# Kernel optimization log

Hardware: AMD Instinct MI355X
Metric: run time of the kernel (lower is better)

Reference implementation:

```python
import jax, jax.numpy as jnp
import numpy as np

N_NODES = 100000
N_EDGES = 800000
VOCAB = 100
D_FEAT = 10
D = 64
EPS = 1e-8  # torch F.cosine_similarity eps


def setup_inputs() -> dict:
    key = jax.random.key(0)
    ks = jax.random.split(key, 8)
    return {
        "nodes": jax.random.randint(ks[0], (N_NODES,), 0, VOCAB),
        "edges": jax.random.randint(ks[1], (N_EDGES, 2), 0, N_NODES),
        "features": jax.random.normal(ks[2], (N_NODES, D_FEAT), dtype=jnp.float32),
        "node_emb": jax.random.normal(ks[3], (VOCAB, D), dtype=jnp.float32),
        "feat_W": jax.random.normal(ks[4], (D, D_FEAT), dtype=jnp.float32) * 0.1,
        "feat_b": jnp.zeros((D,), dtype=jnp.float32),
        "conv1_W": jax.random.normal(ks[5], (D, D), dtype=jnp.float32) * 0.1,
        "conv1_b": jnp.zeros((D,), dtype=jnp.float32),
        "pattern_emb": jax.random.normal(ks[6], (VOCAB, D), dtype=jnp.float32),
        "pattern_id": 42,  # hash(node_type) % 100
    }


def reference(nodes, edges, features, node_emb, feat_W, feat_b,
              conv1_W, conv1_b, pattern_emb, pattern_id):
    # initial embeddings: type embedding + linear feature projection  [N, D]
    embeds = node_emb[nodes] + (features @ feat_W.T + feat_b)

    src, dst = edges[:, 0], edges[:, 1]
    for _ in range(2):  # fixed 2 message-passing rounds (structural loop)
        # scatter-add messages from src to dst (order-independent sum)
        agg = jnp.zeros_like(embeds).at[dst].add(embeds[src])
        embeds = jax.nn.relu((embeds + agg) @ conv1_W.T + conv1_b)

    # cosine similarity of each node embedding against the pattern embedding
    p = pattern_emb[pattern_id]  # [D]
    num = embeds @ p  # [N]
    denom = jnp.maximum(jnp.linalg.norm(embeds, axis=1), EPS) * \
            jnp.maximum(jnp.linalg.norm(p), EPS)
    return num / denom  # [N] match scores
```

## Files before the change

### kernel.cpp

```cpp
#include <hip/hip_runtime.h>
#include <hip/hip_bf16.h>

#define N_NODES 100000
#define N_EDGES 800000
#define D 64
#define SCAN_B 256
#define NB1 ((N_NODES + SCAN_B - 1) / SCAN_B)
#define FILL_BLOCKS (N_EDGES / 256)
#define INIT_BLOCKS (N_NODES * D / 256)
#define CT 64
#define XS 68
#define OS 72

__device__ __forceinline__ unsigned short f2bf(float f) {
    union { float f; unsigned u; } v; v.f = f;
    unsigned r = v.u + 0x7fffu + ((v.u >> 16) & 1u);
    return (unsigned short)(r >> 16);
}
__device__ __forceinline__ float bf2f(unsigned short u) {
    return __uint_as_float(((unsigned)u) << 16);
}
__device__ __forceinline__ void acc_bf8(float acc[8], uint4 u) {
    acc[0] += __uint_as_float(u.x << 16);
    acc[1] += __uint_as_float(u.x & 0xffff0000u);
    acc[2] += __uint_as_float(u.y << 16);
    acc[3] += __uint_as_float(u.y & 0xffff0000u);
    acc[4] += __uint_as_float(u.z << 16);
    acc[5] += __uint_as_float(u.z & 0xffff0000u);
    acc[6] += __uint_as_float(u.w << 16);
    acc[7] += __uint_as_float(u.w & 0xffff0000u);
}
__device__ __forceinline__ unsigned pack2bf(float a, float b) {
    return (unsigned)f2bf(a) | ((unsigned)f2bf(b) << 16);
}

__global__ __launch_bounds__(256) void hist_rank_kernel(
        const int2* __restrict__ edges,
        int* __restrict__ deg,
        int* __restrict__ rank) {
    int t = blockIdx.x * 256 + threadIdx.x;
    int2 e = edges[t];
    rank[t] = atomicAdd(&deg[e.y], 1);
}

__global__ void scan1_kernel(const int* __restrict__ deg,
                             int* __restrict__ row_ptr,
                             int* __restrict__ bsum) {
    __shared__ int tmp[SCAN_B];
    int t = threadIdx.x;
    int i = blockIdx.x * SCAN_B + t;
    int v = (i < N_NODES) ? deg[i] : 0;
    tmp[t] = v;
    __syncthreads();
#pragma unroll
    for (int off = 1; off < SCAN_B; off <<= 1) {
        int a = (t >= off) ? tmp[t - off] : 0;
        __syncthreads();
        tmp[t] += a;
        __syncthreads();
    }
    if (i < N_NODES) row_ptr[i] = tmp[t] - v;
    if (t == SCAN_B - 1) bsum[blockIdx.x] = tmp[t];
}

__global__ void scan23_kernel(int* __restrict__ row_ptr,
                              const int* __restrict__ bsum) {
    __shared__ int red[SCAN_B];
    int t = threadIdx.x;
    int partial = 0;
    if (t < blockIdx.x && t < NB1) partial += bsum[t];
    int t2 = t + 256;
    if (t2 < blockIdx.x && t2 < NB1) partial += bsum[t2];
    red[t] = partial;
    __syncthreads();
#pragma unroll
    for (int off = 128; off > 0; off >>= 1) {
        if (t < off) red[t] += red[t + off];
        __syncthreads();
    }
    int boff = red[0];
    int i = blockIdx.x * SCAN_B + t;
    if (i < N_NODES) row_ptr[i] += boff;
    if (i == 0) row_ptr[N_NODES] = N_EDGES;
}

__global__ __launch_bounds__(256) void fill_init_kernel(
        const int2* __restrict__ edges,
        const int* __restrict__ rank,
        const int* __restrict__ rowp,
        int* __restrict__ col,
        const int* __restrict__ nodes,
        const float* __restrict__ features,
        const float* __restrict__ node_emb,
        const float* __restrict__ feat_W,
        const float* __restrict__ feat_b,
        unsigned short* __restrict__ embeds) {
    if (blockIdx.x < FILL_BLOCKS) {
        int t = blockIdx.x * 256 + threadIdx.x;
        int2 e = edges[t];
        col[rowp[e.y] + rank[t]] = e.x;
    } else {
        int tid = (blockIdx.x - FILL_BLOCKS) * 256 + threadIdx.x;
        int node = tid >> 6;
        int d = tid & 63;
        float acc = feat_b[d];
        const float* f = features + (size_t)node * 10;
        const float* w = feat_W + (size_t)d * 10;
#pragma unroll
        for (int j = 0; j < 10; ++j) acc += f[j] * w[j];
        embeds[tid] = f2bf(node_emb[(size_t)nodes[node] * D + d] + acc);
    }
}

__global__ __launch_bounds__(256, 8) void gather_x_kernel(
        const unsigned short* __restrict__ emb_in,
        const int* __restrict__ rowp,
        const int* __restrict__ col,
        unsigned short* __restrict__ x_out) {
    int lane = threadIdx.x & 63;
    int wv   = threadIdx.x >> 6;
    int node = blockIdx.x * 4 + wv;
    int g = lane >> 3;
    int c = lane & 7;

    int start = rowp[node];
    int end   = rowp[node + 1];

    float acc[8];
#pragma unroll
    for (int j = 0; j < 8; ++j) acc[j] = 0.f;
    if (g == 0) {
        uint4 u = ((const uint4*)(emb_in + (size_t)node * D))[c];
        acc_bf8(acc, u);
    }

    for (int base = start; base < end; base += 32) {
        int nb = end - base; if (nb > 32) nb = 32;
        int idx = (lane < nb) ? col[base + lane] : 0;
#pragma unroll
        for (int r = 0; r < 4; ++r) {
            int s = r * 8 + g;
            int src = __shfl(idx, s, 64);
            if (s < nb) {
                uint4 u = ((const uint4*)(emb_in + (size_t)src * D))[c];
                acc_bf8(acc, u);
            }
        }
    }

#pragma unroll
    for (int m = 8; m <= 32; m <<= 1) {
#pragma unroll
        for (int j = 0; j < 8; ++j) acc[j] += __shfl_xor(acc[j], m, 64);
    }

    if (g == 0) {
        uint4 p;
        p.x = pack2bf(acc[0], acc[1]);
        p.y = pack2bf(acc[2], acc[3]);
        p.z = pack2bf(acc[4], acc[5]);
        p.w = pack2bf(acc[6], acc[7]);
        ((uint4*)(x_out + (size_t)node * D))[c] = p;
    }
}

template <bool SCORE>
__global__ __launch_bounds__(256) void conv_tile_kernel(
        const unsigned short* __restrict__ x,
        const float* __restrict__ W,
        const float* __restrict__ b,
        const float* __restrict__ pattern_emb,
        const int* __restrict__ pattern_id,
        unsigned short* __restrict__ emb_out,
        float* __restrict__ score_out) {
    __shared__ float Xs[CT][XS];
    __shared__ float Wsh[D][XS];
    __shared__ unsigned short Os[CT][OS];
    __shared__ float ps[D];

    int t = threadIdx.x;
    int base = blockIdx.x * CT;
    int i = t & 15;
    int j = t >> 4;

    float bj[4];
#pragma unroll
    for (int dj = 0; dj < 4; ++dj) bj[dj] = b[j + 16 * dj];

    {
        int c = t & 15;
        int r0 = t >> 4;
#pragma unroll
        for (int p4 = 0; p4 < 4; ++p4) {
            int r = r0 + p4 * 16;
            float4 wv4 = ((const float4*)(W + (size_t)r * D))[c];
            *((float4*)&Wsh[r][4 * c]) = wv4;
        }
    }
#pragma unroll
    for (int q = 0; q < 2; ++q) {
        int idx = t + q * 256;
        int r = idx >> 3, ck = idx & 7;
        int node = base + r;
        int nc = node < N_NODES ? node : (N_NODES - 1);
        uint4 u = ((const uint4*)(x + (size_t)nc * D))[ck];
        float4 a, bb;
        a.x  = bf2f((unsigned short)(u.x & 0xffff)); a.y  = bf2f((unsigned short)(u.x >> 16));
        a.z  = bf2f((unsigned short)(u.y & 0xffff)); a.w  = bf2f((unsigned short)(u.y >> 16));
        bb.x = bf2f((unsigned short)(u.z & 0xffff)); bb.y = bf2f((unsigned short)(u.z >> 16));
        bb.z = bf2f((unsigned short)(u.w & 0xffff)); bb.w = bf2f((unsigned short)(u.w >> 16));
        *((float4*)&Xs[r][8 * ck])     = a;
        *((float4*)&Xs[r][8 * ck + 4]) = bb;
    }
    if (SCORE && t < D) ps[t] = pattern_emb[(size_t)pattern_id[0] * D + t];
    __syncthreads();

    float acc[4][4] = {};
    for (int k4 = 0; k4 < 16; ++k4) {
        float4 xr[4], wr[4];
#pragma unroll
        for (int di = 0; di < 4; ++di) xr[di] = *((const float4*)&Xs[i + 16 * di][4 * k4]);
#pragma unroll
        for (int dj = 0; dj < 4; ++dj) wr[dj] = *((const float4*)&Wsh[j + 16 * dj][4 * k4]);
#pragma unroll
        for (int di = 0; di < 4; ++di)
#pragma unroll
            for (int dj = 0; dj < 4; ++dj)
                acc[di][dj] += xr[di].x * wr[dj].x + xr[di].y * wr[dj].y
                             + xr[di].z * wr[dj].z + xr[di].w * wr[dj].w;
    }

    if (!SCORE) {
#pragma unroll
        for (int di = 0; di < 4; ++di)
#pragma unroll
            for (int dj = 0; dj < 4; ++dj)
                Os[i + 16 * di][j + 16 * dj] = f2bf(fmaxf(acc[di][dj] + bj[dj], 0.f));
        __syncthreads();
#pragma unroll
        for (int q = 0; q < 2; ++q) {
            int idx = t + q * 256;
            int r = idx >> 3, seg = idx & 7;
            int node = base + r;
            if (node < N_NODES)
                ((uint4*)(emb_out + (size_t)node * D))[seg] = *((const uint4*)&Os[r][8 * seg]);
        }
    } else {
        __syncthreads();
#pragma unroll
        for (int di = 0; di < 4; ++di)
#pragma unroll
            for (int dj = 0; dj < 4; ++dj)
                Xs[i + 16 * di][j + 16 * dj] = fmaxf(acc[di][dj] + bj[dj], 0.f);
        __syncthreads();
        if (t < CT) {
            float dot = 0.f, n2 = 0.f, pn = 0.f;
#pragma unroll 8
            for (int k = 0; k < D; ++k) {
                float yk = Xs[t][k];
                float pk = ps[k];
                dot += yk * pk; n2 += yk * yk; pn += pk * pk;
            }
            int node = base + t;
            if (node < N_NODES)
                score_out[node] = dot / (fmaxf(sqrtf(n2), 1e-8f) * fmaxf(sqrtf(pn), 1e-8f));
        }
    }
}

__global__ void init_embeds_kernel(const int* __restrict__ nodes,
                                   const float* __restrict__ features,
                                   const float* __restrict__ node_emb,
                                   const float* __restrict__ feat_W,
                                   const float* __restrict__ feat_b,
                                   float* __restrict__ embeds) {
    int tid = blockIdx.x * blockDim.x + threadIdx.x;
    if (tid >= N_NODES * D) return;
    int node = tid >> 6;
    int d = tid & 63;
    float acc = feat_b[d];
    const float* f = features + (size_t)node * 10;
    const float* w = feat_W + (size_t)d * 10;
#pragma unroll
    for (int j = 0; j < 10; ++j) acc += f[j] * w[j];
    embeds[tid] = node_emb[(size_t)nodes[node] * D + d] + acc;
}

__global__ void scatter_add_kernel(const int* __restrict__ edges,
                                   const float* __restrict__ embeds,
                                   float* __restrict__ agg) {
    int tid = blockIdx.x * blockDim.x + threadIdx.x;
    int edge = tid >> 6;
    int lane = tid & 63;
    if (edge >= N_EDGES) return;
    int src = edges[2 * edge + 0];
    int dst = edges[2 * edge + 1];
    atomicAdd(&agg[(size_t)dst * D + lane], embeds[(size_t)src * D + lane]);
}

__global__ void conv_inplace_kernel(const float* __restrict__ agg,
                                    const float* __restrict__ W,
                                    const float* __restrict__ b,
                                    float* __restrict__ embeds) {
    __shared__ float Ws[D * 65];
    __shared__ float xs[4][D];
    for (int i = threadIdx.x; i < D * D; i += blockDim.x) {
        int d = i >> 6, k = i & 63;
        Ws[d * 65 + k] = W[i];
    }
    __syncthreads();
    int lane_d = threadIdx.x & 63;
    int local_n = threadIdx.x >> 6;
    float bias = b[lane_d];
    const int n_chunks = (N_NODES + 3) / 4;
    for (int chunk = blockIdx.x; chunk < n_chunks; chunk += gridDim.x) {
        int node = chunk * 4 + local_n;
        if (node < N_NODES) {
            size_t base = (size_t)node * D + lane_d;
            xs[local_n][lane_d] = embeds[base] + agg[base];
        }
        __syncthreads();
        if (node < N_NODES) {
            float acc = bias;
#pragma unroll
            for (int k = 0; k < D; ++k) acc += xs[local_n][k] * Ws[lane_d * 65 + k];
            embeds[(size_t)node * D + lane_d] = fmaxf(acc, 0.0f);
        }
        __syncthreads();
    }
}

__global__ void final_score_kernel(const float* __restrict__ embeds,
                                   const float* __restrict__ pattern_emb,
                                   const int* __restrict__ pattern_id,
                                   float* __restrict__ out) {
    int lane = threadIdx.x & 63;
    int wave = threadIdx.x >> 6;
    int node = blockIdx.x * 4 + wave;
    int pid = pattern_id[0];
    float p = pattern_emb[(size_t)pid * D + lane];
    float pn = p * p;
#pragma unroll
    for (int m = 32; m > 0; m >>= 1) pn += __shfl_xor(pn, m, 64);
    if (node < N_NODES) {
        float e = embeds[(size_t)node * D + lane];
        float dot = e * p;
        float n2 = e * e;
#pragma unroll
        for (int m = 32; m > 0; m >>= 1) {
            dot += __shfl_xor(dot, m, 64);
            n2  += __shfl_xor(n2, m, 64);
        }
        if (lane == 0) {
            float denom = fmaxf(sqrtf(n2), 1e-8f) * fmaxf(sqrtf(pn), 1e-8f);
            out[node] = dot / denom;
        }
    }
}

extern "C" void kernel_launch(void* const* d_in, const int* in_sizes, int n_in,
                              void* d_out, int out_size, void* d_ws, size_t ws_size,
                              hipStream_t stream) {
    const int*   nodes       = (const int*)d_in[0];
    const int*   edges       = (const int*)d_in[1];
    const float* features    = (const float*)d_in[2];
    const float* node_emb    = (const float*)d_in[3];
    const float* feat_W      = (const float*)d_in[4];
    const float* feat_b      = (const float*)d_in[5];
    const float* conv1_W     = (const float*)d_in[6];
    const float* conv1_b     = (const float*)d_in[7];
    const float* pattern_emb = (const float*)d_in[8];
    const int*   pattern_id  = (const int*)d_in[9];
    float* out = (float*)d_out;

    const size_t emb_f32_bytes = (size_t)N_NODES * D * sizeof(float);
    const size_t emb_bf_bytes  = (size_t)N_NODES * D * 2;
    auto align256 = [](size_t x) { return (x + 255) & ~(size_t)255; };

    size_t o_embA = 0;
    size_t o_embB = o_embA + align256(emb_bf_bytes);
    size_t o_xbuf = o_embB + align256(emb_bf_bytes);
    size_t o_col  = o_xbuf + align256(emb_bf_bytes);
    size_t o_rank = o_col  + align256((size_t)N_EDGES * 4);
    size_t o_row  = o_rank + align256((size_t)N_EDGES * 4);
    size_t o_deg  = o_row  + align256((size_t)(N_NODES + 1) * 4);
    size_t o_bsum = o_deg  + align256((size_t)N_NODES * 4);
    size_t need   = o_bsum + align256((size_t)NB1 * 4);

    char* ws = (char*)d_ws;

    if (ws_size >= need) {
        unsigned short* embA = (unsigned short*)(ws + o_embA);
        unsigned short* embB = (unsigned short*)(ws + o_embB);
        unsigned short* xbuf = (unsigned short*)(ws + o_xbuf);
        int*   col  = (int*)(ws + o_col);
        int*   rank = (int*)(ws + o_rank);
        int*   rowp = (int*)(ws + o_row);
        int*   deg  = (int*)(ws + o_deg);
        int*   bsum = (int*)(ws + o_bsum);

        hipMemsetAsync(deg, 0, (size_t)N_NODES * 4, stream);
        hist_rank_kernel<<<FILL_BLOCKS, 256, 0, stream>>>((const int2*)edges, deg, rank);
        scan1_kernel<<<NB1, SCAN_B, 0, stream>>>(deg, rowp, bsum);
        scan23_kernel<<<NB1, SCAN_B, 0, stream>>>(rowp, bsum);
        fill_init_kernel<<<FILL_BLOCKS + INIT_BLOCKS, 256, 0, stream>>>(
            (const int2*)edges, rank, rowp, col,
            nodes, features, node_emb, feat_W, feat_b, embA);

        const int conv_grid = (N_NODES + CT - 1) / CT;

        gather_x_kernel<<<N_NODES / 4, 256, 0, stream>>>(embA, rowp, col, xbuf);
        conv_tile_kernel<false><<<conv_grid, 256, 0, stream>>>(
            xbuf, conv1_W, conv1_b, pattern_emb, pattern_id, embB, nullptr);
        gather_x_kernel<<<N_NODES / 4, 256, 0, stream>>>(embB, rowp, col, xbuf);
        conv_tile_kernel<true><<<conv_grid, 256, 0, stream>>>(
            xbuf, conv1_W, conv1_b, pattern_emb, pattern_id, nullptr, out);
    } else {
        float* embeds = (float*)ws;
        float* agg = (float*)(ws + align256(emb_f32_bytes));
        init_embeds_kernel<<<(N_NODES * D + 255) / 256, 256, 0, stream>>>(
            nodes, features, node_emb, feat_W, feat_b, embeds);
        for (int it = 0; it < 2; ++it) {
            hipMemsetAsync(agg, 0, emb_f32_bytes, stream);
            long long total = (long long)N_EDGES * 64;
            scatter_add_kernel<<<(int)((total + 255) / 256), 256, 0, stream>>>(edges, embeds, agg);
            conv_inplace_kernel<<<2048, 256, 0, stream>>>(agg, conv1_W, conv1_b, embeds);
        }
        final_score_kernel<<<(N_NODES + 3) / 4, 256, 0, stream>>>(
            embeds, pattern_emb, pattern_id, out);
    }
}
```

Baseline: 256.6 us.

## Fuse neighbor gather with conv tile into a single gconv kernel

Merges the CSR gather-aggregate kernel and the 64x64 conv tile kernel into one 512-thread kernel. Each wave aggregates 8 nodes straight into shared memory as fp32, and the block then runs the dense transform. This removes the bf16 intermediate buffer round trip, two kernel launches per forward pass, and the bf16 rounding of the aggregate. In exchange, the per-block gather runs serially over 8 nodes per wave with load imbalance across waves, and the weight tile and output staging now share a shared-memory union.

Result: slower. 278.0 us (+8.3%).

```diff
diff --git a/kernel.cpp b/kernel.cpp
--- a/kernel.cpp
+++ b/kernel.cpp
@@ -29,9 +29,6 @@
     acc[5] += __uint_as_float(u.z & 0xffff0000u);
     acc[6] += __uint_as_float(u.w << 16);
     acc[7] += __uint_as_float(u.w & 0xffff0000u);
-}
-__device__ __forceinline__ unsigned pack2bf(float a, float b) {
-    return (unsigned)f2bf(a) | ((unsigned)f2bf(b) << 16);
 }
 
 __global__ __launch_bounds__(256) void hist_rank_kernel(
@@ -112,61 +109,11 @@
     }
 }
 
-__global__ __launch_bounds__(256, 8) void gather_x_kernel(
+template <bool SCORE>
+__global__ __launch_bounds__(512, 8) void gconv_kernel(
         const unsigned short* __restrict__ emb_in,
         const int* __restrict__ rowp,
         const int* __restrict__ col,
-        unsigned short* __restrict__ x_out) {
-    int lane = threadIdx.x & 63;
-    int wv   = threadIdx.x >> 6;
-    int node = blockIdx.x * 4 + wv;
-    int g = lane >> 3;
-    int c = lane & 7;
-
-    int start = rowp[node];
-    int end   = rowp[node + 1];
-
-    float acc[8];
-#pragma unroll
-    for (int j = 0; j < 8; ++j) acc[j] = 0.f;
-    if (g == 0) {
-        uint4 u = ((const uint4*)(emb_in + (size_t)node * D))[c];
-        acc_bf8(acc, u);
-    }
-
-    for (int base = start; base < end; base += 32) {
-        int nb = end - base; if (nb > 32) nb = 32;
-        int idx = (lane < nb) ? col[base + lane] : 0;
-#pragma unroll
-        for (int r = 0; r < 4; ++r) {
-            int s = r * 8 + g;
-            int src = __shfl(idx, s, 64);
-            if (s < nb) {
-                uint4 u = ((const uint4*)(emb_in + (size_t)src * D))[c];
-                acc_bf8(acc, u);
-            }
-        }
-    }
-
-#pragma unroll
-    for (int m = 8; m <= 32; m <<= 1) {
-#pragma unroll
-        for (int j = 0; j < 8; ++j) acc[j] += __shfl_xor(acc[j], m, 64);
-    }
-
-    if (g == 0) {
-        uint4 p;
-        p.x = pack2bf(acc[0], acc[1]);
-        p.y = pack2bf(acc[2], acc[3]);
-        p.z = pack2bf(acc[4], acc[5]);
-        p.w = pack2bf(acc[6], acc[7]);
-        ((uint4*)(x_out + (size_t)node * D))[c] = p;
-    }
-}
-
-template <bool SCORE>
-__global__ __launch_bounds__(256) void conv_tile_kernel(
-        const unsigned short* __restrict__ x,
         const float* __restrict__ W,
         const float* __restrict__ b,
         const float* __restrict__ pattern_emb,
@@ -174,84 +121,114 @@
         unsigned short* __restrict__ emb_out,
         float* __restrict__ score_out) {
     __shared__ float Xs[CT][XS];
-    __shared__ float Wsh[D][XS];
-    __shared__ unsigned short Os[CT][OS];
+    __shared__ union {
+        float W4[CT][XS];
+        unsigned short Os[CT][OS];
+    } u;
     __shared__ float ps[D];
 
     int t = threadIdx.x;
     int base = blockIdx.x * CT;
+    int lane = t & 63;
+    int wv = t >> 6;
+
+    {
+        int c = t & 15;
+        int r = t >> 4;
+#pragma unroll
+        for (int p = 0; p < 2; ++p) {
+            int rr = r + 32 * p;
+            *((float4*)&u.W4[rr][4 * c]) = ((const float4*)(W + (size_t)rr * D))[c];
+        }
+    }
+    if (SCORE && t < D) ps[t] = pattern_emb[(size_t)pattern_id[0] * D + t];
+
+    int g = lane >> 3;
+    int c8 = lane & 7;
+    int rp = 0;
+    if (lane <= 8) {
+        int nidx = base + wv * 8 + lane;
+        rp = rowp[nidx <= N_NODES ? nidx : N_NODES];
+    }
+
+    for (int nn = 0; nn < 8; ++nn) {
+        int rl = wv * 8 + nn;
+        int node = base + rl;
+        int start = __shfl(rp, nn, 64);
+        int end   = __shfl(rp, nn + 1, 64);
+
+        float acc[8];
+#pragma unroll
+        for (int j = 0; j < 8; ++j) acc[j] = 0.f;
+        if (g == 0 && node < N_NODES) {
+            uint4 uu = ((const uint4*)(emb_in + (size_t)node * D))[c8];
+            acc_bf8(acc, uu);
+        }
+
+        for (int b2 = start; b2 < end; b2 += 32) {
+            int nb = end - b2; if (nb > 32) nb = 32;
+            int idx = (lane < nb) ? col[b2 + lane] : 0;
+#pragma unroll
+            for (int r = 0; r < 4; ++r) {
+                int s = r * 8 + g;
+                int src = __shfl(idx, s, 64);
+                if (s < nb) {
+                    uint4 uu = ((const uint4*)(emb_in + (size_t)src * D))[c8];
+                    acc_bf8(acc, uu);
+                }
+            }
+        }
+
+#pragma unroll
+        for (int m = 8; m <= 32; m <<= 1)
+#pragma unroll
+            for (int j = 0; j < 8; ++j) acc[j] += __shfl_xor(acc[j], m, 64);
+
+        if (g == 0) {
+            *((float4*)&Xs[rl][8 * c8])     = make_float4(acc[0], acc[1], acc[2], acc[3]);
+            *((float4*)&Xs[rl][8 * c8 + 4]) = make_float4(acc[4], acc[5], acc[6], acc[7]);
+        }
+    }
+    __syncthreads();
+
     int i = t & 15;
     int j = t >> 4;
-
-    float bj[4];
-#pragma unroll
-    for (int dj = 0; dj < 4; ++dj) bj[dj] = b[j + 16 * dj];
-
-    {
-        int c = t & 15;
-        int r0 = t >> 4;
-#pragma unroll
-        for (int p4 = 0; p4 < 4; ++p4) {
-            int r = r0 + p4 * 16;
-            float4 wv4 = ((const float4*)(W + (size_t)r * D))[c];
-            *((float4*)&Wsh[r][4 * c]) = wv4;
-        }
-    }
-#pragma unroll
-    for (int q = 0; q < 2; ++q) {
-        int idx = t + q * 256;
-        int r = idx >> 3, ck = idx & 7;
+    float bj0 = b[j], bj1 = b[j + 32];
+
+    float acc2[4][2] = {};
+    for (int k4 = 0; k4 < 16; ++k4) {
+        float4 xr[4], wr[2];
+#pragma unroll
+        for (int di = 0; di < 4; ++di) xr[di] = *((const float4*)&Xs[i + 16 * di][4 * k4]);
+        wr[0] = *((const float4*)&u.W4[j][4 * k4]);
+        wr[1] = *((const float4*)&u.W4[j + 32][4 * k4]);
+#pragma unroll
+        for (int di = 0; di < 4; ++di)
+#pragma unroll
+            for (int dj = 0; dj < 2; ++dj)
+                acc2[di][dj] += xr[di].x * wr[dj].x + xr[di].y * wr[dj].y
+                              + xr[di].z * wr[dj].z + xr[di].w * wr[dj].w;
+    }
+
+    if (!SCORE) {
+        __syncthreads();
+#pragma unroll
+        for (int di = 0; di < 4; ++di) {
+            u.Os[i + 16 * di][j]      = f2bf(fmaxf(acc2[di][0] + bj0, 0.f));
+            u.Os[i + 16 * di][j + 32] = f2bf(fmaxf(acc2[di][1] + bj1, 0.f));
+        }
+        __syncthreads();
+        int r = t >> 3, seg = t & 7;
         int node = base + r;
-        int nc = node < N_NODES ? node : (N_NODES - 1);
-        uint4 u = ((const uint4*)(x + (size_t)nc * D))[ck];
-        float4 a, bb;
-        a.x  = bf2f((unsigned short)(u.x & 0xffff)); a.y  = bf2f((unsigned short)(u.x >> 16));
-        a.z  = bf2f((unsigned short)(u.y & 0xffff)); a.w  = bf2f((unsigned short)(u.y >> 16));
-        bb.x = bf2f((unsigned short)(u.z & 0xffff)); bb.y = bf2f((unsigned short)(u.z >> 16));
-        bb.z = bf2f((unsigned short)(u.w & 0xffff)); bb.w = bf2f((unsigned short)(u.w >> 16));
-        *((float4*)&Xs[r][8 * ck])     = a;
-        *((float4*)&Xs[r][8 * ck + 4]) = bb;
-    }
-    if (SCORE && t < D) ps[t] = pattern_emb[(size_t)pattern_id[0] * D + t];
-    __syncthreads();
-
-    float acc[4][4] = {};
-    for (int k4 = 0; k4 < 16; ++k4) {
-        float4 xr[4], wr[4];
-#pragma unroll
-        for (int di = 0; di < 4; ++di) xr[di] = *((const float4*)&Xs[i + 16 * di][4 * k4]);
-#pragma unroll
-        for (int dj = 0; dj < 4; ++dj) wr[dj] = *((const float4*)&Wsh[j + 16 * dj][4 * k4]);
-#pragma unroll
-        for (int di = 0; di < 4; ++di)
-#pragma unroll
-            for (int dj = 0; dj < 4; ++dj)
-                acc[di][dj] += xr[di].x * wr[dj].x + xr[di].y * wr[dj].y
-                             + xr[di].z * wr[dj].z + xr[di].w * wr[dj].w;
-    }
-
-    if (!SCORE) {
-#pragma unroll
-        for (int di = 0; di < 4; ++di)
-#pragma unroll
-            for (int dj = 0; dj < 4; ++dj)
-                Os[i + 16 * di][j + 16 * dj] = f2bf(fmaxf(acc[di][dj] + bj[dj], 0.f));
-        __syncthreads();
-#pragma unroll
-        for (int q = 0; q < 2; ++q) {
-            int idx = t + q * 256;
-            int r = idx >> 3, seg = idx & 7;
-            int node = base + r;
-            if (node < N_NODES)
-                ((uint4*)(emb_out + (size_t)node * D))[seg] = *((const uint4*)&Os[r][8 * seg]);
-        }
+        if (node < N_NODES)
+            ((uint4*)(emb_out + (size_t)node * D))[seg] = *((const uint4*)&u.Os[r][8 * seg]);
     } else {
         __syncthreads();
 #pragma unroll
-        for (int di = 0; di < 4; ++di)
-#pragma unroll
-            for (int dj = 0; dj < 4; ++dj)
-                Xs[i + 16 * di][j + 16 * dj] = fmaxf(acc[di][dj] + bj[dj], 0.f);
+        for (int di = 0; di < 4; ++di) {
+            Xs[i + 16 * di][j]      = fmaxf(acc2[di][0] + bj0, 0.f);
+            Xs[i + 16 * di][j + 32] = fmaxf(acc2[di][1] + bj1, 0.f);
+        }
         __syncthreads();
         if (t < CT) {
             float dot = 0.f, n2 = 0.f, pn = 0.f;
@@ -379,8 +356,7 @@
 
     size_t o_embA = 0;
     size_t o_embB = o_embA + align256(emb_bf_bytes);
-    size_t o_xbuf = o_embB + align256(emb_bf_bytes);
-    size_t o_col  = o_xbuf + align256(emb_bf_bytes);
+    size_t o_col  = o_embB + align256(emb_bf_bytes);
     size_t o_rank = o_col  + align256((size_t)N_EDGES * 4);
     size_t o_row  = o_rank + align256((size_t)N_EDGES * 4);
     size_t o_deg  = o_row  + align256((size_t)(N_NODES + 1) * 4);
@@ -392,7 +368,6 @@
     if (ws_size >= need) {
         unsigned short* embA = (unsigned short*)(ws + o_embA);
         unsigned short* embB = (unsigned short*)(ws + o_embB);
-        unsigned short* xbuf = (unsigned short*)(ws + o_xbuf);
         int*   col  = (int*)(ws + o_col);
         int*   rank = (int*)(ws + o_rank);
         int*   rowp = (int*)(ws + o_row);
@@ -409,12 +384,10 @@
 
         const int conv_grid = (N_NODES + CT - 1) / CT;
 
-        gather_x_kernel<<<N_NODES / 4, 256, 0, stream>>>(embA, rowp, col, xbuf);
-        conv_tile_kernel<false><<<conv_grid, 256, 0, stream>>>(
-            xbuf, conv1_W, conv1_b, pattern_emb, pattern_id, embB, nullptr);
-        gather_x_kernel<<<N_NODES / 4, 256, 0, stream>>>(embB, rowp, col, xbuf);
-        conv_tile_kernel<true><<<conv_grid, 256, 0, stream>>>(
-            xbuf, conv1_W, conv1_b, pattern_emb, pattern_id, nullptr, out);
+        gconv_kernel<false><<<conv_grid, 512, 0, stream>>>(
+            embA, rowp, col, conv1_W, conv1_b, pattern_emb, pattern_id, embB, nullptr);
+        gconv_kernel<true><<<conv_grid, 512, 0, stream>>>(
+            embB, rowp, col, conv1_W, conv1_b, pattern_emb, pattern_id, nullptr, out);
     } else {
         float* embeds = (float*)ws;
         float* agg = (float*)(ws + align256(emb_f32_bytes));
```

## Use bf16 MFMA with split-weight precision for conv and atomic-cursor CSR fill

Applied to the files above, without the earlier changes.

Replaces the scalar FP32 shared-memory tiled 64x64 linear layer with MFMA 16x16x32 bf16 instructions. The weights are split into hi and lo bf16 parts, precomputed in an extra block of the fill kernel, so precision stays close to fp32 weights. Also removes the per-edge rank array: CSR fill now takes slots with atomicAdd on a cursor array, which cuts memory traffic but makes the neighbor order nondeterministic. Out-of-range nodes in the last tile are read without clamping, which relies on the workspace slack after xbuf.

After: 297.2 us. 15.8% more time.

```diff
diff --git a/kernel.cpp b/kernel.cpp
--- a/kernel.cpp
+++ b/kernel.cpp
@@ -12,6 +12,9 @@
 #define XS 68
 #define OS 72
 
+using bf16x8 = __attribute__((ext_vector_type(8))) short;
+using f32x4  = __attribute__((ext_vector_type(4))) float;
+
 __device__ __forceinline__ unsigned short f2bf(float f) {
     union { float f; unsigned u; } v; v.f = f;
     unsigned r = v.u + 0x7fffu + ((v.u >> 16) & 1u);
@@ -34,13 +37,12 @@
     return (unsigned)f2bf(a) | ((unsigned)f2bf(b) << 16);
 }
 
-__global__ __launch_bounds__(256) void hist_rank_kernel(
+__global__ __launch_bounds__(256) void hist_kernel(
         const int2* __restrict__ edges,
-        int* __restrict__ deg,
-        int* __restrict__ rank) {
+        int* __restrict__ deg) {
     int t = blockIdx.x * 256 + threadIdx.x;
     int2 e = edges[t];
-    rank[t] = atomicAdd(&deg[e.y], 1);
+    atomicAdd(&deg[e.y], 1);
 }
 
 __global__ void scan1_kernel(const int* __restrict__ deg,
@@ -64,7 +66,8 @@
 }
 
 __global__ void scan23_kernel(int* __restrict__ row_ptr,
-                              const int* __restrict__ bsum) {
+                              const int* __restrict__ bsum,
+                              int* __restrict__ cursor) {
     __shared__ int red[SCAN_B];
     int t = threadIdx.x;
     int partial = 0;
@@ -80,26 +83,32 @@
     }
     int boff = red[0];
     int i = blockIdx.x * SCAN_B + t;
-    if (i < N_NODES) row_ptr[i] += boff;
+    if (i < N_NODES) {
+        int v = row_ptr[i] + boff;
+        row_ptr[i] = v;
+        cursor[i] = v;
+    }
     if (i == 0) row_ptr[N_NODES] = N_EDGES;
 }
 
 __global__ __launch_bounds__(256) void fill_init_kernel(
         const int2* __restrict__ edges,
-        const int* __restrict__ rank,
-        const int* __restrict__ rowp,
+        int* __restrict__ cursor,
         int* __restrict__ col,
         const int* __restrict__ nodes,
         const float* __restrict__ features,
         const float* __restrict__ node_emb,
         const float* __restrict__ feat_W,
         const float* __restrict__ feat_b,
-        unsigned short* __restrict__ embeds) {
+        unsigned short* __restrict__ embeds,
+        const float* __restrict__ conv1_W,
+        unsigned short* __restrict__ Whi,
+        unsigned short* __restrict__ Wlo) {
     if (blockIdx.x < FILL_BLOCKS) {
         int t = blockIdx.x * 256 + threadIdx.x;
         int2 e = edges[t];
-        col[rowp[e.y] + rank[t]] = e.x;
-    } else {
+        col[atomicAdd(&cursor[e.y], 1)] = e.x;
+    } else if (blockIdx.x < FILL_BLOCKS + INIT_BLOCKS) {
         int tid = (blockIdx.x - FILL_BLOCKS) * 256 + threadIdx.x;
         int node = tid >> 6;
         int d = tid & 63;
@@ -109,6 +118,16 @@
 #pragma unroll
         for (int j = 0; j < 10; ++j) acc += f[j] * w[j];
         embeds[tid] = f2bf(node_emb[(size_t)nodes[node] * D + d] + acc);
+    } else {
+        int t = threadIdx.x;
+#pragma unroll
+        for (int j = 0; j < 16; ++j) {
+            int i = t + 256 * j;
+            float w = conv1_W[i];
+            unsigned short hi = f2bf(w);
+            Whi[i] = hi;
+            Wlo[i] = f2bf(w - bf2f(hi));
+        }
     }
 }
 
@@ -165,77 +184,56 @@
 }
 
 template <bool SCORE>
-__global__ __launch_bounds__(256) void conv_tile_kernel(
+__global__ __launch_bounds__(256) void conv_mfma_kernel(
         const unsigned short* __restrict__ x,
-        const float* __restrict__ W,
+        const unsigned short* __restrict__ Whi,
+        const unsigned short* __restrict__ Wlo,
         const float* __restrict__ b,
         const float* __restrict__ pattern_emb,
         const int* __restrict__ pattern_id,
         unsigned short* __restrict__ emb_out,
         float* __restrict__ score_out) {
-    __shared__ float Xs[CT][XS];
-    __shared__ float Wsh[D][XS];
-    __shared__ unsigned short Os[CT][OS];
+    __shared__ union {
+        unsigned short Os[CT][OS];
+        float Ys[CT][XS];
+    } u;
     __shared__ float ps[D];
 
     int t = threadIdx.x;
+    int lane = t & 63;
+    int wv = t >> 6;
     int base = blockIdx.x * CT;
-    int i = t & 15;
-    int j = t >> 4;
-
+    int nodebase = base + wv * 16;
+    int row16 = lane & 15;
+    int kq = lane >> 4;
+
+    if (SCORE && t < D) ps[t] = pattern_emb[(size_t)pattern_id[0] * D + t];
+
+    const bf16x8* xp = (const bf16x8*)(x + (size_t)(nodebase + row16) * D + kq * 8);
+    bf16x8 a0 = xp[0];
+    bf16x8 a1 = xp[4];
+
+    f32x4 acc[4] = {};
     float bj[4];
 #pragma unroll
-    for (int dj = 0; dj < 4; ++dj) bj[dj] = b[j + 16 * dj];
-
-    {
-        int c = t & 15;
-        int r0 = t >> 4;
-#pragma unroll
-        for (int p4 = 0; p4 < 4; ++p4) {
-            int r = r0 + p4 * 16;
-            float4 wv4 = ((const float4*)(W + (size_t)r * D))[c];
-            *((float4*)&Wsh[r][4 * c]) = wv4;
-        }
-    }
-#pragma unroll
-    for (int q = 0; q < 2; ++q) {
-        int idx = t + q * 256;
-        int r = idx >> 3, ck = idx & 7;
-        int node = base + r;
-        int nc = node < N_NODES ? node : (N_NODES - 1);
-        uint4 u = ((const uint4*)(x + (size_t)nc * D))[ck];
-        float4 a, bb;
-        a.x  = bf2f((unsigned short)(u.x & 0xffff)); a.y  = bf2f((unsigned short)(u.x >> 16));
-        a.z  = bf2f((unsigned short)(u.y & 0xffff)); a.w  = bf2f((unsigned short)(u.y >> 16));
-        bb.x = bf2f((unsigned short)(u.z & 0xffff)); bb.y = bf2f((unsigned short)(u.z >> 16));
-        bb.z = bf2f((unsigned short)(u.w & 0xffff)); bb.w = bf2f((unsigned short)(u.w >> 16));
-        *((float4*)&Xs[r][8 * ck])     = a;
-        *((float4*)&Xs[r][8 * ck + 4]) = bb;
-    }
-    if (SCORE && t < D) ps[t] = pattern_emb[(size_t)pattern_id[0] * D + t];
-    __syncthreads();
-
-    float acc[4][4] = {};
-    for (int k4 = 0; k4 < 16; ++k4) {
-        float4 xr[4], wr[4];
-#pragma unroll
-        for (int di = 0; di < 4; ++di) xr[di] = *((const float4*)&Xs[i + 16 * di][4 * k4]);
-#pragma unroll
-        for (int dj = 0; dj < 4; ++dj) wr[dj] = *((const float4*)&Wsh[j + 16 * dj][4 * k4]);
-#pragma unroll
-        for (int di = 0; di < 4; ++di)
-#pragma unroll
-            for (int dj = 0; dj < 4; ++dj)
-                acc[di][dj] += xr[di].x * wr[dj].x + xr[di].y * wr[dj].y
-                             + xr[di].z * wr[dj].z + xr[di].w * wr[dj].w;
+    for (int tc = 0; tc < 4; ++tc) {
+        int o = tc * 16 + row16;
+        bj[tc] = b[o];
+        const bf16x8* wh = (const bf16x8*)(Whi + (size_t)o * D + kq * 8);
+        const bf16x8* wl = (const bf16x8*)(Wlo + (size_t)o * D + kq * 8);
+        acc[tc] = __builtin_amdgcn_mfma_f32_16x16x32_bf16(a0, wh[0], acc[tc], 0, 0, 0);
+        acc[tc] = __builtin_amdgcn_mfma_f32_16x16x32_bf16(a1, wh[4], acc[tc], 0, 0, 0);
+        acc[tc] = __builtin_amdgcn_mfma_f32_16x16x32_bf16(a0, wl[0], acc[tc], 0, 0, 0);
+        acc[tc] = __builtin_amdgcn_mfma_f32_16x16x32_bf16(a1, wl[4], acc[tc], 0, 0, 0);
     }
 
     if (!SCORE) {
 #pragma unroll
-        for (int di = 0; di < 4; ++di)
-#pragma unroll
-            for (int dj = 0; dj < 4; ++dj)
-                Os[i + 16 * di][j + 16 * dj] = f2bf(fmaxf(acc[di][dj] + bj[dj], 0.f));
+        for (int tc = 0; tc < 4; ++tc)
+#pragma unroll
+            for (int r = 0; r < 4; ++r)
+                u.Os[wv * 16 + kq * 4 + r][tc * 16 + row16] =
+                    f2bf(fmaxf(acc[tc][r] + bj[tc], 0.f));
         __syncthreads();
 #pragma unroll
         for (int q = 0; q < 2; ++q) {
@@ -243,21 +241,20 @@
             int r = idx >> 3, seg = idx & 7;
             int node = base + r;
             if (node < N_NODES)
-                ((uint4*)(emb_out + (size_t)node * D))[seg] = *((const uint4*)&Os[r][8 * seg]);
+                ((uint4*)(emb_out + (size_t)node * D))[seg] = *((const uint4*)&u.Os[r][8 * seg]);
         }
     } else {
-        __syncthreads();
-#pragma unroll
-        for (int di = 0; di < 4; ++di)
-#pragma unroll
-            for (int dj = 0; dj < 4; ++dj)
-                Xs[i + 16 * di][j + 16 * dj] = fmaxf(acc[di][dj] + bj[dj], 0.f);
+#pragma unroll
+        for (int tc = 0; tc < 4; ++tc)
+#pragma unroll
+            for (int r = 0; r < 4; ++r)
+                u.Ys[wv * 16 + kq * 4 + r][tc * 16 + row16] = fmaxf(acc[tc][r] + bj[tc], 0.f);
         __syncthreads();
         if (t < CT) {
             float dot = 0.f, n2 = 0.f, pn = 0.f;
 #pragma unroll 8
             for (int k = 0; k < D; ++k) {
-                float yk = Xs[t][k];
+                float yk = u.Ys[t][k];
                 float pk = ps[k];
                 dot += yk * pk; n2 += yk * yk; pn += pk * pk;
             }
@@ -381,11 +378,13 @@
     size_t o_embB = o_embA + align256(emb_bf_bytes);
     size_t o_xbuf = o_embB + align256(emb_bf_bytes);
     size_t o_col  = o_xbuf + align256(emb_bf_bytes);
-    size_t o_rank = o_col  + align256((size_t)N_EDGES * 4);
-    size_t o_row  = o_rank + align256((size_t)N_EDGES * 4);
-    size_t o_deg  = o_row  + align256((size_t)(N_NODES + 1) * 4);
+    size_t o_row  = o_col  + align256((size_t)N_EDGES * 4);
+    size_t o_cur  = o_row  + align256((size_t)(N_NODES + 1) * 4);
+    size_t o_deg  = o_cur  + align256((size_t)N_NODES * 4);
     size_t o_bsum = o_deg  + align256((size_t)N_NODES * 4);
-    size_t need   = o_bsum + align256((size_t)NB1 * 4);
+    size_t o_whi  = o_bsum + align256((size_t)NB1 * 4);
+    size_t o_wlo  = o_whi  + align256((size_t)D * D * 2);
+    size_t need   = o_wlo  + align256((size_t)D * D * 2);
 
     char* ws = (char*)d_ws;
 
@@ -394,27 +393,30 @@
         unsigned short* embB = (unsigned short*)(ws + o_embB);
         unsigned short* xbuf = (unsigned short*)(ws + o_xbuf);
         int*   col  = (int*)(ws + o_col);
-        int*   rank = (int*)(ws + o_rank);
         int*   rowp = (int*)(ws + o_row);
+        int*   cur  = (int*)(ws + o_cur);
         int*   deg  = (int*)(ws + o_deg);
         int*   bsum = (int*)(ws + o_bsum);
+        unsigned short* Whi = (unsigned short*)(ws + o_whi);
+        unsigned short* Wlo = (unsigned short*)(ws + o_wlo);
 
         hipMemsetAsync(deg, 0, (size_t)N_NODES * 4, stream);
-        hist_rank_kernel<<<FILL_BLOCKS, 256, 0, stream>>>((const int2*)edges, deg, rank);
+        hist_kernel<<<FILL_BLOCKS, 256, 0, stream>>>((const int2*)edges, deg);
         scan1_kernel<<<NB1, SCAN_B, 0, stream>>>(deg, rowp, bsum);
-        scan23_kernel<<<NB1, SCAN_B, 0, stream>>>(rowp, bsum);
-        fill_init_kernel<<<FILL_BLOCKS + INIT_BLOCKS, 256, 0, stream>>>(
-            (const int2*)edges, rank, rowp, col,
-            nodes, features, node_emb, feat_W, feat_b, embA);
+        scan23_kernel<<<NB1, SCAN_B, 0, stream>>>(rowp, bsum, cur);
+        fill_init_kernel<<<FILL_BLOCKS + INIT_BLOCKS + 1, 256, 0, stream>>>(
+            (const int2*)edges, cur, col,
+            nodes, features, node_emb, feat_W, feat_b, embA,
+            conv1_W, Whi, Wlo);
 
         const int conv_grid = (N_NODES + CT - 1) / CT;
 
         gather_x_kernel<<<N_NODES / 4, 256, 0, stream>>>(embA, rowp, col, xbuf);
-        conv_tile_kernel<false><<<conv_grid, 256, 0, stream>>>(
-            xbuf, conv1_W, conv1_b, pattern_emb, pattern_id, embB, nullptr);
+        conv_mfma_kernel<false><<<conv_grid, 256, 0, stream>>>(
+            xbuf, Whi, Wlo, conv1_b, pattern_emb, pattern_id, embB, nullptr);
         gather_x_kernel<<<N_NODES / 4, 256, 0, stream>>>(embB, rowp, col, xbuf);
-        conv_tile_kernel<true><<<conv_grid, 256, 0, stream>>>(
-            xbuf, conv1_W, conv1_b, pattern_emb, pattern_id, nullptr, out);
+        conv_mfma_kernel<true><<<conv_grid, 256, 0, stream>>>(
+            xbuf, Whi, Wlo, conv1_b, pattern_emb, pattern_id, nullptr, out);
     } else {
         float* embeds = (float*)ws;
         float* agg = (float*)(ws + align256(emb_f32_bytes));
```
